# Optimization experiments

Measured on AMD Instinct MI355X. Metric: run time of the kernel, lower is better.

Reference implementation:

```python
import jax, jax.numpy as jnp
import numpy as np

D_MODEL = 768
D_STATE = 16
D_CONV = 4
EXPAND = 2
D_INNER = EXPAND * D_MODEL  # 1536
BATCH = 2
SEQLEN = 4096


def setup_inputs() -> dict:
    key = jax.random.key(0)
    ks = jax.random.split(key, 8)
    s = 0.02
    return {
        "hidden_states": jax.random.normal(ks[0], (BATCH, SEQLEN, D_MODEL), jnp.float32),
        "W_in": jax.random.normal(ks[1], (D_MODEL, 2 * D_INNER), jnp.float32) * s,
        "conv_w": jax.random.normal(ks[2], (D_INNER, 1, D_CONV), jnp.float32) * s,
        "conv_b": jnp.zeros((D_INNER,), jnp.float32),
        "W_x": jax.random.normal(ks[3], (D_INNER, 2 * D_STATE + D_INNER), jnp.float32) * s,
        "W_dt": jax.random.normal(ks[4], (D_INNER, D_INNER), jnp.float32) * s,
        "b_dt": jnp.zeros((D_INNER,), jnp.float32),
        "A_log": jax.random.uniform(ks[5], (D_INNER, D_STATE), jnp.float32, minval=-1.0, maxval=0.0),
        "D": jnp.ones((D_INNER,), jnp.float32),
        "W_out": jax.random.normal(ks[6], (D_INNER, D_MODEL), jnp.float32) * s,
    }


def _silu(x):
    return x * jax.nn.sigmoid(x)


def reference(hidden_states, W_in, conv_w, conv_b, W_x, W_dt, b_dt, A_log, D, W_out):
    B, L, _ = hidden_states.shape
    # in_proj and split into x / gate z  (torch splits first half -> x, second -> z)
    xz = hidden_states @ W_in                      # (B, L, 2*ed)
    x, z = xz[..., :D_INNER], xz[..., D_INNER:]
    # causal depthwise conv1d (torch pads d_conv-1 both sides then truncates to L == left pad)
    xc = jnp.swapaxes(x, 1, 2)                     # (B, ed, L)
    xc = jax.lax.conv_general_dilated(
        xc, conv_w, window_strides=(1,), padding=[(D_CONV - 1, 0)],
        dimension_numbers=("NCH", "OIH", "NCH"), feature_group_count=D_INNER)
    x = jnp.swapaxes(xc, 1, 2) + conv_b            # (B, L, ed)
    x = _silu(x)
    # input-dependent SSM params
    xp = x @ W_x                                   # (B, L, 2*ds + ed)
    Bm = jax.nn.softmax(xp[..., :D_STATE], axis=-1)          # (B, L, ds)
    Cm = xp[..., D_STATE:2 * D_STATE]                          # (B, L, ds)
    delta = jax.nn.softplus(xp[..., 2 * D_STATE:] @ W_dt + b_dt)  # (B, L, ed)
    A = -jnp.exp(A_log.astype(jnp.float32))        # (ed, ds)

    def step(h, t):
        dt, Bt, Ct, ut = t                         # (B,ed),(B,ds),(B,ds),(B,ed)
        dA = jnp.exp(dt[:, :, None] * A)           # (B, ed, ds)
        h = dA * h + (dt[:, :, None] * Bt[:, None, :]) * ut[:, :, None]
        y = jnp.einsum('bs,bds->bd', Ct, h)        # (B, ed)
        return h, y

    h0 = jnp.zeros((B, D_INNER, D_STATE), x.dtype)
    ts = (jnp.swapaxes(delta, 0, 1), jnp.swapaxes(Bm, 0, 1),
          jnp.swapaxes(Cm, 0, 1), jnp.swapaxes(x, 0, 1))
    _, ys = jax.lax.scan(step, h0, ts)             # ys: (L, B, ed)
    y = jnp.swapaxes(ys, 0, 1)                     # (B, L, ed)
    # gating + out projection (torch fallback path does NOT add D * u)
    y = y * _silu(z)
    return y @ W_out
```

## Files before the change

### kernel.cpp

```cpp
#include <hip/hip_runtime.h>
#include <hip/hip_bf16.h>
#include <math.h>

#define D_MODEL 768
#define D_STATE 16
#define D_CONVW 4
#define D_INNER 1536
#define BATCH   2
#define SEQLEN  4096
#define NROWS   (BATCH*SEQLEN)
#define NCHUNK  128
#define LCHUNK  (SEQLEN/NCHUNK)

typedef __attribute__((ext_vector_type(8))) short short8;
typedef __attribute__((ext_vector_type(4))) float floatx4;

__device__ inline unsigned short f2b(float x) {
    unsigned u = __float_as_uint(x);
    return (unsigned short)((u + 0x7fffu + ((u >> 16) & 1u)) >> 16);
}
__device__ inline float b2f(unsigned short b) {
    return __uint_as_float(((unsigned)b) << 16);
}

#define GLDS(gp, lp) __builtin_amdgcn_global_load_lds( \
    (const __attribute__((address_space(1))) void*)(gp), \
    (__attribute__((address_space(3))) void*)(lp), 16, 0, 0)

template<int EPI, int OUTBF16>
__global__ __launch_bounds__(256, 4) void gemm_p2(
    const unsigned short* __restrict__ A, int lda,
    const unsigned short* __restrict__ Bt, int ldb,
    void* __restrict__ Cv, int ldc, float* __restrict__ C2,
    int N, int K, const float* __restrict__ bias, int nbx)
{
    __shared__ unsigned short As0[128*32], As1[128*32];
    __shared__ unsigned short Bs0[128*32], Bs1[128*32];

    const int nwg = gridDim.x;
    const int cpx = nwg >> 3;
    const int wg  = blockIdx.x;
    const int xcd = wg & 7, local = wg >> 3;
    int bmi, bni;
    if ((cpx % nbx == 0) && ((nbx & 1) == 0)) {
        const int R   = cpx / nbx;
        const int p   = local / (2 * R);
        const int idx = local % (2 * R);
        bmi = xcd * R + (idx >> 1);
        bni = p * 2 + (idx & 1);
    } else {
        const int swz = xcd * cpx + local;
        bmi = swz / nbx;
        bni = swz % nbx;
    }
    const int bm = bmi * 128;
    const int bn = bni * 128;

    const int tid  = threadIdx.x;
    const int lane = tid & 63;
    const int wave = tid >> 6;
    const int wm   = (wave >> 1) * 64;
    const int wn   = (wave & 1) * 64;
    const int l15  = lane & 15;
    const int lg   = lane >> 4;

    const int sr    = tid >> 2;
    const int sg    = ((tid & 3) ^ ((tid >> 3) & 3)) * 8;
    const int lbase = (tid & ~63) * 16;

    floatx4 acc[4][4] = {};

    auto stagePair = [&](unsigned short (&SA)[128*32],
                         unsigned short (&SB)[128*32], int kt) {
        #pragma unroll
        for (int p = 0; p < 2; ++p) {
            const unsigned short* ga = A + (size_t)(bm + p * 64 + sr) * lda + kt + sg;
            GLDS(ga, (char*)SA + p * 4096 + lbase);
        }
        #pragma unroll
        for (int p = 0; p < 2; ++p) {
            const unsigned short* gb = Bt + (size_t)(bn + p * 64 + sr) * ldb + kt + sg;
            GLDS(gb, (char*)SB + p * 4096 + lbase);
        }
    };

    auto compute = [&](const unsigned short (&CA)[128*32],
                       const unsigned short (&CB)[128*32]) {
        short8 af[4], bfv[4];
        #pragma unroll
        for (int i = 0; i < 4; ++i) {
            const int tr = wm + i * 16 + l15;
            const int ge = lg ^ ((tr >> 1) & 3);
            af[i] = *(const short8*)((const char*)CA + tr * 64 + ge * 16);
        }
        #pragma unroll
        for (int j = 0; j < 4; ++j) {
            const int tr = wn + j * 16 + l15;
            const int ge = lg ^ ((tr >> 1) & 3);
            bfv[j] = *(const short8*)((const char*)CB + tr * 64 + ge * 16);
        }
        #pragma unroll
        for (int i = 0; i < 4; ++i)
            #pragma unroll
            for (int j = 0; j < 4; ++j)
                acc[i][j] = __builtin_amdgcn_mfma_f32_16x16x32_bf16(
                    af[i], bfv[j], acc[i][j], 0, 0, 0);
    };

    const int NT = K >> 5;

    stagePair(As0, Bs0, 0);

    #define STEP(SA, SB, CA, CB, T)                                          \
    {                                                                        \
        const int t_ = (T);                                                  \
        if (t_ + 1 < NT) {                                                   \
            stagePair(SA, SB, (t_ + 1) * 32);                                \
            asm volatile("s_waitcnt vmcnt(4)" ::: "memory");                 \
        } else {                                                             \
            asm volatile("s_waitcnt vmcnt(0)" ::: "memory");                 \
        }                                                                    \
        __builtin_amdgcn_sched_barrier(0);                                   \
        __builtin_amdgcn_s_barrier();                                        \
        __builtin_amdgcn_sched_barrier(0);                                   \
        compute(CA, CB);                                                     \
        __builtin_amdgcn_sched_barrier(0);                                   \
        __builtin_amdgcn_s_barrier();                                        \
        __builtin_amdgcn_sched_barrier(0);                                   \
    }

    for (int t = 0; t < NT; t += 2) {
        STEP(As1, Bs1, As0, Bs0, t);
        STEP(As0, Bs0, As1, Bs1, t + 1);
    }
    #undef STEP

    #pragma unroll
    for (int i = 0; i < 4; ++i) {
        #pragma unroll
        for (int r = 0; r < 4; ++r) {
            const int gm = bm + wm + i * 16 + lg * 4 + r;
            #pragma unroll
            for (int j = 0; j < 4; ++j) {
                const int gn = bn + wn + j * 16 + l15;
                float v = acc[i][j][r];
                if (EPI == 1) {
                    if (gn < N) {
                        v += bias[gn];
                        v = (v > 20.f) ? v : log1pf(__expf(v));
                        ((float*)Cv)[(size_t)gm * ldc + gn] = v;
                    }
                } else if (EPI == 3) {
                    if (gn < 32) {
                        C2[(size_t)gm * 32 + gn] = v;
                    } else if (gn < N) {
                        v += bias[gn - 32];
                        v = (v > 20.f) ? v : log1pf(__expf(v));
                        ((float*)Cv)[(size_t)gm * 1536 + gn - 32] = v;
                    }
                } else {
                    if (gn < N) {
                        if (OUTBF16)
                            ((unsigned short*)Cv)[(size_t)gm * ldc + gn] = f2b(v);
                        else
                            ((float*)Cv)[(size_t)gm * ldc + gn] = v;
                    }
                }
            }
        }
    }
}

__global__ __launch_bounds__(256) void transpose_bf16(
    const float* __restrict__ W, unsigned short* __restrict__ Wt, int K, int N)
{
    __shared__ float t[32][33];
    const int nt = blockIdx.x * 32, kt = blockIdx.y * 32;
    const int tx = threadIdx.x & 31, ty = threadIdx.x >> 5;
    #pragma unroll
    for (int r = 0; r < 4; ++r) {
        const int k = ty + r * 8;
        const int n = nt + tx;
        float v = 0.f;
        if (n < N) v = W[(size_t)(kt + k) * N + n];
        t[k][tx] = v;
    }
    __syncthreads();
    #pragma unroll
    for (int r = 0; r < 4; ++r) {
        const int nl = ty + r * 8;
        Wt[(size_t)(nt + nl) * K + kt + tx] = f2b(t[tx][nl]);
    }
}

__global__ __launch_bounds__(256) void f32_to_bf16(
    const float* __restrict__ in, unsigned short* __restrict__ o, int n4)
{
    const int i = blockIdx.x * 256 + threadIdx.x;
    if (i >= n4) return;
    float4 v = ((const float4*)in)[i];
    ushort4 r;
    r.x = f2b(v.x); r.y = f2b(v.y); r.z = f2b(v.z); r.w = f2b(v.w);
    ((ushort4*)o)[i] = r;
}

__global__ __launch_bounds__(256) void wx32_to_bf16(
    const float* __restrict__ Wx, unsigned short* __restrict__ o)
{
    const int i = blockIdx.x * 256 + threadIdx.x;
    if (i >= 1536 * 384) return;
    const int row = i / 384, q = i % 384;
    float4 v = *(const float4*)(Wx + (size_t)row * 1568 + 32 + q * 4);
    ushort4 r;
    r.x = f2b(v.x); r.y = f2b(v.y); r.z = f2b(v.z); r.w = f2b(v.w);
    *(ushort4*)(o + (size_t)row * 1536 + q * 4) = r;
}

__global__ __launch_bounds__(256) void conv_silu8(
    const unsigned short* __restrict__ xzb, const float* __restrict__ w,
    const float* __restrict__ cb, unsigned short* __restrict__ ub)
{
    const int i = blockIdx.x * 256 + threadIdx.x;
    if (i >= NROWS * 192) return;
    const int g   = i % 192;
    const int row = i / 192;
    const int l   = row % SEQLEN;
    const int d0  = g * 8;

    short8 xr[4];
    #pragma unroll
    for (int k = 0; k < 4; ++k) {
        const int ll = l - 3 + k;
        if (ll >= 0)
            xr[k] = *(const short8*)&xzb[(size_t)(row - 3 + k) * 3072 + d0];
        else
            xr[k] = short8{0,0,0,0,0,0,0,0};
    }
    unsigned short o[8];
    #pragma unroll
    for (int e = 0; e < 8; ++e) {
        float4 we = *(const float4*)&w[(d0 + e) * 4];
        float a = cb[d0 + e];
        a = fmaf(b2f((unsigned short)xr[0][e]), we.x, a);
        a = fmaf(b2f((unsigned short)xr[1][e]), we.y, a);
        a = fmaf(b2f((unsigned short)xr[2][e]), we.z, a);
        a = fmaf(b2f((unsigned short)xr[3][e]), we.w, a);
        o[e] = f2b(a / (1.f + __expf(-a)));
    }
    *(short8*)&ub[(size_t)row * 1536 + d0] = *(short8*)o;
}

__global__ __launch_bounds__(256) void softmax_bc_kernel(
    const float* __restrict__ xp32, float* __restrict__ Bsm, float* __restrict__ Csm)
{
    const int row = blockIdx.x * 256 + threadIdx.x;
    if (row >= NROWS) return;
    const float* p = xp32 + (size_t)row * 32;
    float v[16];
    #pragma unroll
    for (int q = 0; q < 4; ++q) {
        float4 t = *(const float4*)(p + q * 4);
        v[q*4+0]=t.x; v[q*4+1]=t.y; v[q*4+2]=t.z; v[q*4+3]=t.w;
    }
    float mx = v[0];
    #pragma unroll
    for (int s = 1; s < 16; ++s) mx = fmaxf(mx, v[s]);
    float sum = 0.f;
    #pragma unroll
    for (int s = 0; s < 16; ++s) { v[s] = __expf(v[s] - mx); sum += v[s]; }
    const float inv = 1.f / sum;
    float* bo = Bsm + (size_t)row * 16;
    float* co = Csm + (size_t)row * 16;
    #pragma unroll
    for (int s = 0; s < 16; ++s) bo[s] = v[s] * inv;
    #pragma unroll
    for (int q = 0; q < 4; ++q)
        *(float4*)(co + q * 4) = *(const float4*)(p + 16 + q * 4);
}

__global__ __launch_bounds__(256) void scan_chunk_state(
    const float* __restrict__ delta, const unsigned short* __restrict__ ub,
    const float* __restrict__ Bsm, const float* __restrict__ A_log,
    float* __restrict__ chunkS, float* __restrict__ dtsum)
{
    const int gid = blockIdx.x * 256 + threadIdx.x;
    const int d = gid % D_INNER;
    const int c = (gid / D_INNER) % NCHUNK;
    const int b = gid / (D_INNER * NCHUNK);

    float A2[16];
    #pragma unroll
    for (int q = 0; q < 4; ++q) {
        float4 t = *(const float4*)(A_log + d * 16 + q * 4);
        A2[q*4+0] = -__expf(t.x) * 1.44269504089f;
        A2[q*4+1] = -__expf(t.y) * 1.44269504089f;
        A2[q*4+2] = -__expf(t.z) * 1.44269504089f;
        A2[q*4+3] = -__expf(t.w) * 1.44269504089f;
    }
    float h[16];
    #pragma unroll
    for (int s = 0; s < 16; ++s) h[s] = 0.f;
    float dts = 0.f;

    const int t0 = c * LCHUNK;
    for (int t = t0; t < t0 + LCHUNK; ++t) {
        const size_t rowoff = (size_t)b * SEQLEN + t;
        const float dt = delta[rowoff * D_INNER + d];
        const float uu = b2f(ub[rowoff * D_INNER + d]);
        const float du = dt * uu;
        dts += dt;
        const float4* Bp = (const float4*)(Bsm + rowoff * 16);
        float Bv[16];
        #pragma unroll
        for (int q = 0; q < 4; ++q) {
            float4 tb = Bp[q];
            Bv[q*4+0]=tb.x; Bv[q*4+1]=tb.y; Bv[q*4+2]=tb.z; Bv[q*4+3]=tb.w;
        }
        #pragma unroll
        for (int s = 0; s < 16; ++s) {
            const float dA = exp2f(dt * A2[s]);
            h[s] = fmaf(dA, h[s], du * Bv[s]);
        }
    }
    float* S = chunkS + (size_t)gid * 16;
    #pragma unroll
    for (int q = 0; q < 4; ++q)
        *(float4*)(S + q * 4) = make_float4(h[q*4+0], h[q*4+1], h[q*4+2], h[q*4+3]);
    dtsum[gid] = dts;
}

__global__ __launch_bounds__(256) void scan_chunk_scan(
    const float* __restrict__ A_log, const float* __restrict__ dtsum,
    float* __restrict__ chunkS)
{
    const int gid = blockIdx.x * 256 + threadIdx.x;
    if (gid >= BATCH * D_INNER * 16) return;
    const int s = gid % 16;
    const int d = (gid / 16) % D_INNER;
    const int b = gid / (16 * D_INNER);
    const float A2 = -__expf(A_log[d * 16 + s]) * 1.44269504089f;
    float hprev = 0.f;
    for (int c = 0; c < NCHUNK; ++c) {
        const size_t cidx = ((size_t)(b * NCHUNK + c) * D_INNER + d);
        const float P  = exp2f(A2 * dtsum[cidx]);
        const size_t idx = cidx * 16 + s;
        const float Sc = chunkS[idx];
        chunkS[idx] = hprev;
        hprev = fmaf(P, hprev, Sc);
    }
}

__global__ __launch_bounds__(256) void scan_output(
    const float* __restrict__ delta, const unsigned short* __restrict__ ub,
    const float* __restrict__ Bsm, const float* __restrict__ Csm,
    const float* __restrict__ A_log, const float* __restrict__ chunkS,
    const unsigned short* __restrict__ xzb, unsigned short* __restrict__ yb)
{
    const int gid = blockIdx.x * 256 + threadIdx.x;
    const int d = gid % D_INNER;
    const int c = (gid / D_INNER) % NCHUNK;
    const int b = gid / (D_INNER * NCHUNK);

    float A2[16];
    #pragma unroll
    for (int q = 0; q < 4; ++q) {
        float4 t = *(const float4*)(A_log + d * 16 + q * 4);
        A2[q*4+0] = -__expf(t.x) * 1.44269504089f;
        A2[q*4+1] = -__expf(t.y) * 1.44269504089f;
        A2[q*4+2] = -__expf(t.z) * 1.44269504089f;
        A2[q*4+3] = -__expf(t.w) * 1.44269504089f;
    }
    float h[16];
    const float* S = chunkS + (size_t)gid * 16;
    #pragma unroll
    for (int q = 0; q < 4; ++q) {
        float4 t = *(const float4*)(S + q * 4);
        h[q*4+0]=t.x; h[q*4+1]=t.y; h[q*4+2]=t.z; h[q*4+3]=t.w;
    }

    const int t0 = c * LCHUNK;
    for (int t = t0; t < t0 + LCHUNK; ++t) {
        const size_t rowoff = (size_t)b * SEQLEN + t;
        const float dt = delta[rowoff * D_INNER + d];
        const float uu = b2f(ub[rowoff * D_INNER + d]);
        const float du = dt * uu;
        const float4* Bp = (const float4*)(Bsm + rowoff * 16);
        const float4* Cp = (const float4*)(Csm + rowoff * 16);
        float Bv[16], Cv[16];
        #pragma unroll
        for (int q = 0; q < 4; ++q) {
            float4 tb = Bp[q], tc = Cp[q];
            Bv[q*4+0]=tb.x; Bv[q*4+1]=tb.y; Bv[q*4+2]=tb.z; Bv[q*4+3]=tb.w;
            Cv[q*4+0]=tc.x; Cv[q*4+1]=tc.y; Cv[q*4+2]=tc.z; Cv[q*4+3]=tc.w;
        }
        float yv = 0.f;
        #pragma unroll
        for (int s = 0; s < 16; ++s) {
            const float dA = exp2f(dt * A2[s]);
            h[s] = fmaf(dA, h[s], du * Bv[s]);
            yv = fmaf(Cv[s], h[s], yv);
        }
        const float z = b2f(xzb[rowoff * (2 * D_INNER) + D_INNER + d]);
        const float sz = z / (1.f + __expf(-z));
        yb[rowoff * D_INNER + d] = f2b(yv * sz);
    }
}

extern "C" void kernel_launch(void* const* d_in, const int* in_sizes, int n_in,
                              void* d_out, int out_size, void* d_ws, size_t ws_size,
                              hipStream_t stream)
{
    const float* hs     = (const float*)d_in[0];
    const float* W_in   = (const float*)d_in[1];
    const float* conv_w = (const float*)d_in[2];
    const float* conv_b = (const float*)d_in[3];
    const float* W_x    = (const float*)d_in[4];
    const float* W_dt   = (const float*)d_in[5];
    const float* b_dt   = (const float*)d_in[6];
    const float* A_log  = (const float*)d_in[7];
    const float* W_out  = (const float*)d_in[9];
    float* out = (float*)d_out;

    char* w = (char*)d_ws;
    auto alloc = [&](size_t bytes) { char* p = w; w += (bytes + 255) & ~(size_t)255; return p; };
    float*          xp32   = (float*)alloc((size_t)NROWS * 32 * 4);
    float*          delta  = (float*)alloc((size_t)NROWS * 1536 * 4);
    float*          Bsm    = (float*)alloc((size_t)NROWS * 16 * 4);
    float*          Csm    = (float*)alloc((size_t)NROWS * 16 * 4);
    float*          chunkS = (float*)alloc((size_t)BATCH * NCHUNK * D_INNER * 16 * 4);
    float*          dtsum  = (float*)alloc((size_t)BATCH * NCHUNK * D_INNER * 4);
    unsigned short* xzb    = (unsigned short*)alloc((size_t)NROWS * 3072 * 2);
    unsigned short* ub     = (unsigned short*)alloc((size_t)NROWS * 1536 * 2);
    unsigned short* yb     = (unsigned short*)alloc((size_t)NROWS * 1536 * 2);
    unsigned short* hsb    = (unsigned short*)alloc((size_t)NROWS * 768 * 2);
    unsigned short* Wt_in  = (unsigned short*)alloc((size_t)3072 * 768 * 2);
    unsigned short* Wt_x   = (unsigned short*)alloc((size_t)1792 * 1536 * 2);
    unsigned short* Wt_dt  = (unsigned short*)alloc((size_t)1536 * 1536 * 2);
    unsigned short* Wt_out = (unsigned short*)alloc((size_t)768 * 1536 * 2);
    unsigned short* wxb    = (unsigned short*)alloc((size_t)1536 * 1536 * 2);

    const dim3 blk(256);

    transpose_bf16<<<dim3(3072/32, 768/32),  blk, 0, stream>>>(W_in,  Wt_in,  768,  3072);
    transpose_bf16<<<dim3(1792/32, 1536/32), blk, 0, stream>>>(W_x,   Wt_x,   1536, 1568);
    transpose_bf16<<<dim3(1536/32, 1536/32), blk, 0, stream>>>(W_dt,  Wt_dt,  1536, 1536);
    transpose_bf16<<<dim3(768/32,  1536/32), blk, 0, stream>>>(W_out, Wt_out, 1536, 768);
    f32_to_bf16<<<(NROWS*768/4 + 255)/256, blk, 0, stream>>>(hs, hsb, NROWS*768/4);
    wx32_to_bf16<<<(1536*384 + 255)/256, blk, 0, stream>>>(W_x, wxb);

    gemm_p2<0,1><<<dim3(144), blk, 0, stream>>>(
        Wt_dt, 1536, wxb, 1536, Wt_x + (size_t)32 * 1536, 1536, nullptr,
        1536, 1536, nullptr, 12);

    gemm_p2<0,1><<<dim3(1536), blk, 0, stream>>>(
        hsb, 768, Wt_in, 768, xzb, 3072, nullptr, 3072, 768, nullptr, 24);

    conv_silu8<<<(NROWS*192)/256, blk, 0, stream>>>(xzb, conv_w, conv_b, ub);

    gemm_p2<3,0><<<dim3(896), blk, 0, stream>>>(
        ub, 1536, Wt_x, 1536, delta, 1536, xp32, 1568, 1536, b_dt, 14);

    softmax_bc_kernel<<<NROWS/256, blk, 0, stream>>>(xp32, Bsm, Csm);

    scan_chunk_state<<<(BATCH*NCHUNK*D_INNER)/256, blk, 0, stream>>>(
        delta, ub, Bsm, A_log, chunkS, dtsum);
    scan_chunk_scan<<<(BATCH*D_INNER*16 + 255)/256, blk, 0, stream>>>(
        A_log, dtsum, chunkS);
    scan_output<<<(BATCH*NCHUNK*D_INNER)/256, blk, 0, stream>>>(
        delta, ub, Bsm, Csm, A_log, chunkS, xzb, yb);

    gemm_p2<0,0><<<dim3(384), blk, 0, stream>>>(
        yb, 1536, Wt_out, 1536, out, 768, nullptr, 768, 1536, nullptr, 6);
}
```

Measured before the change: 443.8 us.

## Store delta as bf16 and triple-buffer GEMM LDS with one barrier per step

The x_proj/dt GEMM epilogue now writes softplus(delta) as bf16 instead of fp32, and both scan kernels read the bf16 delta. This halves the traffic of the largest intermediate, which is written once and read twice. The GEMM also moves from double to triple LDS buffering, which lets it drop the trailing barrier after each compute step. The costs are lower precision in delta and a larger LDS footprint per block (six 8 KB tiles), which may reduce how many blocks fit on a CU.

After: 500.2 us. +12.7%, slower.

```diff
diff --git a/kernel.cpp b/kernel.cpp
--- a/kernel.cpp
+++ b/kernel.cpp
@@ -28,14 +28,14 @@
     (__attribute__((address_space(3))) void*)(lp), 16, 0, 0)
 
 template<int EPI, int OUTBF16>
-__global__ __launch_bounds__(256, 4) void gemm_p2(
+__global__ __launch_bounds__(256, 4) void gemm_1b(
     const unsigned short* __restrict__ A, int lda,
     const unsigned short* __restrict__ Bt, int ldb,
     void* __restrict__ Cv, int ldc, float* __restrict__ C2,
     int N, int K, const float* __restrict__ bias, int nbx)
 {
-    __shared__ unsigned short As0[128*32], As1[128*32];
-    __shared__ unsigned short Bs0[128*32], Bs1[128*32];
+    __shared__ unsigned short As0[128*32], As1[128*32], As2[128*32];
+    __shared__ unsigned short Bs0[128*32], Bs1[128*32], Bs2[128*32];
 
     const int nwg = gridDim.x;
     const int cpx = nwg >> 3;
@@ -124,14 +124,12 @@
         __builtin_amdgcn_s_barrier();                                        \
         __builtin_amdgcn_sched_barrier(0);                                   \
         compute(CA, CB);                                                     \
-        __builtin_amdgcn_sched_barrier(0);                                   \
-        __builtin_amdgcn_s_barrier();                                        \
-        __builtin_amdgcn_sched_barrier(0);                                   \
-    }
-
-    for (int t = 0; t < NT; t += 2) {
+    }
+
+    for (int t = 0; t < NT; t += 3) {
         STEP(As1, Bs1, As0, Bs0, t);
-        STEP(As0, Bs0, As1, Bs1, t + 1);
+        STEP(As2, Bs2, As1, Bs1, t + 1);
+        STEP(As0, Bs0, As2, Bs2, t + 2);
     }
     #undef STEP
 
@@ -144,19 +142,13 @@
             for (int j = 0; j < 4; ++j) {
                 const int gn = bn + wn + j * 16 + l15;
                 float v = acc[i][j][r];
-                if (EPI == 1) {
-                    if (gn < N) {
-                        v += bias[gn];
-                        v = (v > 20.f) ? v : log1pf(__expf(v));
-                        ((float*)Cv)[(size_t)gm * ldc + gn] = v;
-                    }
-                } else if (EPI == 3) {
+                if (EPI == 3) {
                     if (gn < 32) {
                         C2[(size_t)gm * 32 + gn] = v;
                     } else if (gn < N) {
                         v += bias[gn - 32];
                         v = (v > 20.f) ? v : log1pf(__expf(v));
-                        ((float*)Cv)[(size_t)gm * 1536 + gn - 32] = v;
+                        ((unsigned short*)Cv)[(size_t)gm * 1536 + gn - 32] = f2b(v);
                     }
                 } else {
                     if (gn < N) {
@@ -279,7 +271,7 @@
 }
 
 __global__ __launch_bounds__(256) void scan_chunk_state(
-    const float* __restrict__ delta, const unsigned short* __restrict__ ub,
+    const unsigned short* __restrict__ deltab, const unsigned short* __restrict__ ub,
     const float* __restrict__ Bsm, const float* __restrict__ A_log,
     float* __restrict__ chunkS, float* __restrict__ dtsum)
 {
@@ -305,7 +297,7 @@
     const int t0 = c * LCHUNK;
     for (int t = t0; t < t0 + LCHUNK; ++t) {
         const size_t rowoff = (size_t)b * SEQLEN + t;
-        const float dt = delta[rowoff * D_INNER + d];
+        const float dt = b2f(deltab[rowoff * D_INNER + d]);
         const float uu = b2f(ub[rowoff * D_INNER + d]);
         const float du = dt * uu;
         dts += dt;
@@ -351,7 +343,7 @@
 }
 
 __global__ __launch_bounds__(256) void scan_output(
-    const float* __restrict__ delta, const unsigned short* __restrict__ ub,
+    const unsigned short* __restrict__ deltab, const unsigned short* __restrict__ ub,
     const float* __restrict__ Bsm, const float* __restrict__ Csm,
     const float* __restrict__ A_log, const float* __restrict__ chunkS,
     const unsigned short* __restrict__ xzb, unsigned short* __restrict__ yb)
@@ -381,7 +373,7 @@
     const int t0 = c * LCHUNK;
     for (int t = t0; t < t0 + LCHUNK; ++t) {
         const size_t rowoff = (size_t)b * SEQLEN + t;
-        const float dt = delta[rowoff * D_INNER + d];
+        const float dt = b2f(deltab[rowoff * D_INNER + d]);
         const float uu = b2f(ub[rowoff * D_INNER + d]);
         const float du = dt * uu;
         const float4* Bp = (const float4*)(Bsm + rowoff * 16);
@@ -424,7 +416,7 @@
     char* w = (char*)d_ws;
     auto alloc = [&](size_t bytes) { char* p = w; w += (bytes + 255) & ~(size_t)255; return p; };
     float*          xp32   = (float*)alloc((size_t)NROWS * 32 * 4);
-    float*          delta  = (float*)alloc((size_t)NROWS * 1536 * 4);
+    unsigned short* deltab = (unsigned short*)alloc((size_t)NROWS * 1536 * 2);
     float*          Bsm    = (float*)alloc((size_t)NROWS * 16 * 4);
     float*          Csm    = (float*)alloc((size_t)NROWS * 16 * 4);
     float*          chunkS = (float*)alloc((size_t)BATCH * NCHUNK * D_INNER * 16 * 4);
@@ -448,27 +440,27 @@
     f32_to_bf16<<<(NROWS*768/4 + 255)/256, blk, 0, stream>>>(hs, hsb, NROWS*768/4);
     wx32_to_bf16<<<(1536*384 + 255)/256, blk, 0, stream>>>(W_x, wxb);
 
-    gemm_p2<0,1><<<dim3(144), blk, 0, stream>>>(
+    gemm_1b<0,1><<<dim3(144), blk, 0, stream>>>(
         Wt_dt, 1536, wxb, 1536, Wt_x + (size_t)32 * 1536, 1536, nullptr,
         1536, 1536, nullptr, 12);
 
-    gemm_p2<0,1><<<dim3(1536), blk, 0, stream>>>(
+    gemm_1b<0,1><<<dim3(1536), blk, 0, stream>>>(
         hsb, 768, Wt_in, 768, xzb, 3072, nullptr, 3072, 768, nullptr, 24);
 
     conv_silu8<<<(NROWS*192)/256, blk, 0, stream>>>(xzb, conv_w, conv_b, ub);
 
-    gemm_p2<3,0><<<dim3(896), blk, 0, stream>>>(
-        ub, 1536, Wt_x, 1536, delta, 1536, xp32, 1568, 1536, b_dt, 14);
+    gemm_1b<3,0><<<dim3(896), blk, 0, stream>>>(
+        ub, 1536, Wt_x, 1536, deltab, 1536, xp32, 1568, 1536, b_dt, 14);
 
     softmax_bc_kernel<<<NROWS/256, blk, 0, stream>>>(xp32, Bsm, Csm);
 
     scan_chunk_state<<<(BATCH*NCHUNK*D_INNER)/256, blk, 0, stream>>>(
-        delta, ub, Bsm, A_log, chunkS, dtsum);
+        deltab, ub, Bsm, A_log, chunkS, dtsum);
     scan_chunk_scan<<<(BATCH*D_INNER*16 + 255)/256, blk, 0, stream>>>(
         A_log, dtsum, chunkS);
     scan_output<<<(BATCH*NCHUNK*D_INNER)/256, blk, 0, stream>>>(
-        delta, ub, Bsm, Csm, A_log, chunkS, xzb, yb);
-
-    gemm_p2<0,0><<<dim3(384), blk, 0, stream>>>(
+        deltab, ub, Bsm, Csm, A_log, chunkS, xzb, yb);
+
+    gemm_1b<0,0><<<dim3(384), blk, 0, stream>>>(
         yb, 1536, Wt_out, 1536, out, 768, nullptr, 768, 1536, nullptr, 6);
 }
```
